# Optimization experiments

Measured on AMD Instinct MI355X. Metric: run time of the kernel, lower is better.

The kernel has to match this reference:

```python
import jax, jax.numpy as jnp
import numpy as np

N_NODES = 10000
N_EDGES = 640000
IN_CH, HID, OUT_CH = 128, 128, 64


def _gcn_conv(x, edge_index, edge_weight, W, b, n_nodes):
    # PyG GCNConv (default add_self_loops=True, normalize=True, bias=True):
    #   A_hat = A + I ; D = rowsum(A_hat) ; norm_e = D^-1/2[src] * w_e * D^-1/2[dst]
    #   out[dst] += norm_e * (x @ W)[src] ; out += b
    src, dst = edge_index[0], edge_index[1]
    loop = jnp.arange(n_nodes, dtype=edge_index.dtype)
    src = jnp.concatenate([src, loop])
    dst = jnp.concatenate([dst, loop])
    w = jnp.concatenate([edge_weight, jnp.ones((n_nodes,), edge_weight.dtype)])
    deg = jax.ops.segment_sum(w, dst, num_segments=n_nodes)  # scatter on col
    dinv = jnp.where(deg > 0, jax.lax.rsqrt(deg), 0.0).astype(x.dtype)
    norm = dinv[src] * w * dinv[dst]  # [E+N]
    xw = x @ W  # dense GEMM [N, out]
    msg = norm[:, None] * xw[src]  # gather + scale [E+N, out]
    out = jax.ops.segment_sum(msg, dst, num_segments=n_nodes)  # scatter-add
    return out + b


def setup_inputs() -> dict:
    key = jax.random.key(0)
    ks = jax.random.split(key, 8)
    x = jax.random.normal(ks[0], (N_NODES, IN_CH), dtype=jnp.float32)
    edge_index = jax.random.randint(ks[1], (2, N_EDGES), 0, N_NODES, dtype=jnp.int64)
    edge_weight = jax.random.uniform(ks[2], (N_EDGES,), dtype=jnp.float32)
    W1 = jax.random.normal(ks[3], (IN_CH, HID), dtype=jnp.float32) * 0.05
    b1 = jnp.zeros((HID,), jnp.float32)
    W2 = jax.random.normal(ks[4], (HID, OUT_CH), dtype=jnp.float32) * 0.05
    b2 = jnp.zeros((OUT_CH,), jnp.float32)
    return {"x": x, "edge_index": edge_index, "edge_weight": edge_weight,
            "W1": W1, "b1": b1, "W2": W2, "b2": b2}


def reference(x, edge_index, edge_weight, W1, b1, W2, b2):
    h = _gcn_conv(x, edge_index, edge_weight, W1, b1, N_NODES)
    h = jax.nn.relu(h)
    out = _gcn_conv(h, edge_index, edge_weight, W2, b2, N_NODES)
    return out
```

## Files before the change

kernel.cpp:

```cpp
#include <hip/hip_runtime.h>
#include <math.h>

#define N_NODES 10000
#define N_EDGES 640000
#define K_DIM   128
#define OUT_CH  64
#define ELLW    192

#define CHUNKS  128
#define CHUNK_E 5000
#define GB      313

typedef unsigned long long ull;
typedef unsigned int uint;
typedef unsigned short ushort;
typedef unsigned char uchar;

#define FIXED_SCALE 262144.0f


__device__ __forceinline__ float bf_lo(uint u) {
    return __uint_as_float(u << 16);
}
__device__ __forceinline__ float bf_hi(uint u) {
    return __uint_as_float(u & 0xffff0000u);
}
__device__ __forceinline__ ushort f2bf(float v) {
    uint u = __float_as_uint(v);
    uint r = u + 0x7fffu + ((u >> 16) & 1u);
    return (ushort)(r >> 16);
}

template <int NCOL>
__device__ void gemm_body(const float* __restrict__ A, const float* __restrict__ B,
                          ushort* __restrict__ C, int blk, int M,
                          float* sA , float* sB ) {
    constexpr int K = 128;
    constexpr int TM = 32;
    constexpr int KT = 32;
    constexpr int R = 256 / NCOL;
    constexpr int RPT = TM / R;
    int tid = threadIdx.x;
    int c = tid % NCOL;
    int rr = tid / NCOL;
    int row0 = blk * TM;
    float acc[RPT];
#pragma unroll
    for (int r = 0; r < RPT; ++r) acc[r] = 0.0f;

    for (int k0 = 0; k0 < K; k0 += KT) {
        for (int i = tid; i < TM * KT; i += 256) {
            int r = i / KT, k = i % KT;
            int gr = row0 + r;
            sA[r * (KT + 1) + k] = (gr < M) ? A[gr * K + k0 + k] : 0.0f;
        }
        for (int i = tid; i < KT * NCOL; i += 256) {
            int k = i / NCOL, cc = i % NCOL;
            sB[k * NCOL + cc] = B[(k0 + k) * NCOL + cc];
        }
        __syncthreads();
#pragma unroll
        for (int k = 0; k < KT; ++k) {
            float b = sB[k * NCOL + c];
#pragma unroll
            for (int r = 0; r < RPT; ++r)
                acc[r] += sA[(rr * RPT + r) * (KT + 1) + k] * b;
        }
        __syncthreads();
    }
#pragma unroll
    for (int r = 0; r < RPT; ++r) {
        int gr = row0 + rr * RPT + r;
        if (gr < M) C[gr * NCOL + c] = f2bf(acc[r]);
    }
}

__global__ __launch_bounds__(256) void preA_gemm1_kernel(const int* __restrict__ ei,
                                                         const float* __restrict__ ew,
                                                         uchar* __restrict__ rank8,
                                                         uint* __restrict__ sd32,
                                                         uint* __restrict__ blockcnt,
                                                         const float* __restrict__ x,
                                                         const float* __restrict__ W1,
                                                         ushort* __restrict__ xw1b) {
    __shared__ uint smem[N_NODES];
    if (blockIdx.x < CHUNKS) {
        const int c = blockIdx.x;
        const int tid = threadIdx.x;
        __shared__ int sflag;
        if (tid == 0) sflag = 0;
        for (int i = tid; i < N_NODES; i += 256) smem[i] = 0u;
        __syncthreads();
        int a = (tid < 64) ? ei[2 * (c * CHUNK_E + tid) + 1] : 0;
        if (a) atomicOr(&sflag, 1);
        __syncthreads();
        const int f = sflag;
        const ull* ei64 = (const ull*)ei;
        for (int k = tid; k < CHUNK_E; k += 256) {
            int e = c * CHUNK_E + k;
            int s, d;
            if (f) { s = ei[e];        d = ei[N_EDGES + e]; }
            else   { s = (int)ei64[e]; d = (int)ei64[N_EDGES + e]; }
            float w = ew[e];
            uint fx = (uint)(w * FIXED_SCALE + 0.5f);
            uint old = atomicAdd(&smem[d], (1u << 24) | fx);
            rank8[e] = (uchar)(old >> 24);
            sd32[e] = ((uint)d << 16) | (uint)s;
        }
        __syncthreads();
        for (int i = tid; i < N_NODES; i += 256)
            blockcnt[c * N_NODES + i] = smem[i];
    } else {
        float* sA = (float*)smem;
        float* sB = sA + 32 * 33;
        gemm_body<128>(x, W1, xw1b, blockIdx.x - CHUNKS, N_NODES, sA, sB);
    }
}

__global__ __launch_bounds__(256) void scanB_kernel(const uint* __restrict__ blockcnt,
                                                    uchar* __restrict__ base8,
                                                    int* __restrict__ cnt_arr,
                                                    float* __restrict__ dinv) {
    int n = blockIdx.x * 256 + threadIdx.x;
    if (n >= N_NODES) return;
    uint wsum = 0;
    int run = 0;
#pragma unroll 8
    for (int c = 0; c < CHUNKS; ++c) {
        uint v = blockcnt[c * N_NODES + n];
        base8[c * N_NODES + n] = (uchar)run;
        run += (int)(v >> 24);
        wsum += v & 0xffffffu;
    }
    cnt_arr[n] = run;
    float dg = 1.0f + (float)wsum * (1.0f / FIXED_SCALE);
    dinv[n] = (float)(1.0 / sqrt((double)dg));
}

#define FILL_SPLIT 4
#define FILL_PART  (CHUNK_E / FILL_SPLIT)
__global__ __launch_bounds__(256) void fillC_kernel(const uint* __restrict__ sd32,
                                                    const float* __restrict__ ew,
                                                    const uchar* __restrict__ rank8,
                                                    const uchar* __restrict__ base8,
                                                    const float* __restrict__ dinv,
                                                    ull* __restrict__ epack) {
    const int c = blockIdx.x / FILL_SPLIT;
    const int p = blockIdx.x % FILL_SPLIT;
    const int k0 = p * FILL_PART;
    for (int k = k0 + threadIdx.x; k < k0 + FILL_PART; k += 256) {
        int e = c * CHUNK_E + k;
        uint sd = sd32[e];
        int s = (int)(sd & 0xffffu);
        int d = (int)(sd >> 16);
        float nrm = dinv[s] * ew[e] * dinv[d];
        int slot = (int)base8[c * N_NODES + d] + (int)rank8[e];
        if (slot < ELLW)
            epack[d * ELLW + slot] = ((ull)__float_as_uint(nrm) << 32) | (ull)(uint)s;
    }
}

__global__ __launch_bounds__(256) void gemm2_kernel(const float* __restrict__ A,
                                                    const float* __restrict__ B,
                                                    ushort* __restrict__ C) {
    __shared__ float sA[32 * 33];
    __shared__ float sB[32 * 64];
    gemm_body<64>(A, B, C, blockIdx.x, N_NODES, sA, sB);
}

__global__ __launch_bounds__(64) void agg1_kernel(const ushort* __restrict__ xwb,
                                                  const ull* __restrict__ epack,
                                                  const int* __restrict__ cnt_arr,
                                                  const float* __restrict__ dinv,
                                                  const float* __restrict__ bias,
                                                  float* __restrict__ out) {
    const uint* __restrict__ xw32 = (const uint*)xwb;
    int node = blockIdx.x;
    int l = threadIdx.x;
    int cnt = __builtin_amdgcn_readfirstlane(cnt_arr[node]);
    if (cnt > ELLW) cnt = ELLW;
    float dn = dinv[node];
    float d2 = dn * dn;
    uint su = xw32[node * 64 + l];
    float acc0 = d2 * bf_lo(su);
    float acc1 = d2 * bf_hi(su);
    const ull* ep = epack + (long)node * ELLW;
#pragma unroll 8
    for (int j = 0; j < cnt; ++j) {
        ull v = ep[j];
        uint s = (uint)v;
        float n = __uint_as_float((uint)(v >> 32));
        uint u = xw32[s * 64 + l];
        acc0 = fmaf(n, bf_lo(u), acc0);
        acc1 = fmaf(n, bf_hi(u), acc1);
    }
    float2 bb = ((const float2*)bias)[l];
    float2 o;
    o.x = fmaxf(acc0 + bb.x, 0.0f);
    o.y = fmaxf(acc1 + bb.y, 0.0f);
    ((float2*)out)[node * 64 + l] = o;
}

__global__ __launch_bounds__(64) void agg2_kernel(const ushort* __restrict__ xwb,
                                                  const ull* __restrict__ epack,
                                                  const int* __restrict__ cnt_arr,
                                                  const float* __restrict__ dinv,
                                                  const float* __restrict__ bias,
                                                  float* __restrict__ out) {
    const uint* __restrict__ xw32 = (const uint*)xwb;
    int A = blockIdx.x * 2;
    int B = A + 1;
    int lane = threadIdx.x;
    int half = lane >> 5;
    int q = lane & 31;
    int cntA = __builtin_amdgcn_readfirstlane(cnt_arr[A]);
    int cntB = __builtin_amdgcn_readfirstlane(cnt_arr[B]);
    if (cntA > ELLW) cntA = ELLW;
    if (cntB > ELLW) cntB = ELLW;
    float dnA = dinv[A], dnB = dinv[B];
    int myn = half ? B : A;
    int mycnt = half ? cntB : cntA;
    float dn = half ? dnB : dnA;
    float d2 = dn * dn;
    uint su = xw32[myn * 32 + q];
    float acc0 = d2 * bf_lo(su);
    float acc1 = d2 * bf_hi(su);
    const ull* epA = epack + (long)A * ELLW;
    const ull* epB = epack + (long)B * ELLW;
    int mx = cntA > cntB ? cntA : cntB;
#pragma unroll 4
    for (int j = 0; j < mx; ++j) {
        ull vA = epA[j];
        ull vB = epB[j];
        ull v = half ? vB : vA;
        uint s = (uint)v & 0xffffu;
        float n = (j < mycnt) ? __uint_as_float((uint)(v >> 32)) : 0.0f;
        uint u = xw32[s * 32 + q];
        acc0 = fmaf(n, bf_lo(u), acc0);
        acc1 = fmaf(n, bf_hi(u), acc1);
    }
    float2 bb = ((const float2*)bias)[q];
    float2 o;
    o.x = acc0 + bb.x;
    o.y = acc1 + bb.y;
    ((float2*)out)[myn * 32 + q] = o;
}

extern "C" void kernel_launch(void* const* d_in, const int* in_sizes, int n_in,
                              void* d_out, int out_size, void* d_ws, size_t ws_size,
                              hipStream_t stream) {
    const float* x  = (const float*)d_in[0];
    const int*   ei = (const int*)d_in[1];
    const float* ew = (const float*)d_in[2];
    const float* W1 = (const float*)d_in[3];
    const float* b1 = (const float*)d_in[4];
    const float* W2 = (const float*)d_in[5];
    const float* b2 = (const float*)d_in[6];
    float* out = (float*)d_out;

    char* ws = (char*)d_ws;
    ushort* xw1b    = (ushort*)(ws + 0);
    float*  h       = (float*) (ws + 2560000);
    ushort* xw2b    = (ushort*)(ws + 7680000);
    ull*    epack   = (ull*)   (ws + 8960000);
    uint*   blockcnt= (uint*)  (ws + 24320000);
    uchar*  base8   = (uchar*) (ws + 29440000);
    uchar*  rank8   = (uchar*) (ws + 30720000);
    uint*   sd32    = (uint*)  (ws + 31360000);
    int*    cnt_arr = (int*)   (ws + 33920000);
    float*  dinv    = (float*) (ws + 33960000);

    preA_gemm1_kernel<<<CHUNKS + GB, 256, 0, stream>>>(ei, ew, rank8, sd32, blockcnt, x, W1, xw1b);
    scanB_kernel<<<(N_NODES + 255) / 256, 256, 0, stream>>>(blockcnt, base8, cnt_arr, dinv);
    fillC_kernel<<<CHUNKS * FILL_SPLIT, 256, 0, stream>>>(sd32, ew, rank8, base8, dinv, epack);
    agg1_kernel<<<N_NODES, 64, 0, stream>>>(xw1b, epack, cnt_arr, dinv, b1, h);
    gemm2_kernel<<<GB, 256, 0, stream>>>(h, W2, xw2b);
    agg2_kernel<<<N_NODES / 2, 64, 0, stream>>>(xw2b, epack, cnt_arr, dinv, b2, out);
}
```

Before: 167.9 us.

## Fuse all GCN stages into one persistent kernel with grid barriers

Replaces six kernel launches with a single persistent kernel of 512 blocks that runs every phase (edge counting plus GEMM1, scan, ELL fill, aggregation 1, GEMM2, aggregation 2), separated by atomic-counter grid barriers. It also stores the hidden activations as bf16 instead of fp32 to halve that traffic. The aim is to remove launch gaps and tail effects between stages. In exchange, the grid-stride loops may load-balance worse than per-node blocks, the barriers rely on all 512 blocks being co-resident, and the extra bf16 rounding of the hidden layer adds error.

```diff
diff --git a/kernel.cpp b/kernel.cpp
--- a/kernel.cpp
+++ b/kernel.cpp
@@ -3,13 +3,13 @@
 
 #define N_NODES 10000
 #define N_EDGES 640000
-#define K_DIM   128
 #define OUT_CH  64
 #define ELLW    192
 
 #define CHUNKS  128
 #define CHUNK_E 5000
 #define GB      313
+#define NBLOCKS 512
 
 typedef unsigned long long ull;
 typedef unsigned int uint;
@@ -19,74 +19,42 @@
 #define FIXED_SCALE 262144.0f
 
 
-__device__ __forceinline__ float bf_lo(uint u) {
-    return __uint_as_float(u << 16);
-}
-__device__ __forceinline__ float bf_hi(uint u) {
-    return __uint_as_float(u & 0xffff0000u);
-}
+__device__ __forceinline__ float bf_lo(uint u) { return __uint_as_float(u << 16); }
+__device__ __forceinline__ float bf_hi(uint u) { return __uint_as_float(u & 0xffff0000u); }
 __device__ __forceinline__ ushort f2bf(float v) {
     uint u = __float_as_uint(v);
     uint r = u + 0x7fffu + ((u >> 16) & 1u);
     return (ushort)(r >> 16);
 }
 
-template <int NCOL>
-__device__ void gemm_body(const float* __restrict__ A, const float* __restrict__ B,
-                          ushort* __restrict__ C, int blk, int M,
-                          float* sA , float* sB ) {
-    constexpr int K = 128;
-    constexpr int TM = 32;
-    constexpr int KT = 32;
-    constexpr int R = 256 / NCOL;
-    constexpr int RPT = TM / R;
-    int tid = threadIdx.x;
-    int c = tid % NCOL;
-    int rr = tid / NCOL;
-    int row0 = blk * TM;
-    float acc[RPT];
-#pragma unroll
-    for (int r = 0; r < RPT; ++r) acc[r] = 0.0f;
-
-    for (int k0 = 0; k0 < K; k0 += KT) {
-        for (int i = tid; i < TM * KT; i += 256) {
-            int r = i / KT, k = i % KT;
-            int gr = row0 + r;
-            sA[r * (KT + 1) + k] = (gr < M) ? A[gr * K + k0 + k] : 0.0f;
-        }
-        for (int i = tid; i < KT * NCOL; i += 256) {
-            int k = i / NCOL, cc = i % NCOL;
-            sB[k * NCOL + cc] = B[(k0 + k) * NCOL + cc];
-        }
-        __syncthreads();
-#pragma unroll
-        for (int k = 0; k < KT; ++k) {
-            float b = sB[k * NCOL + c];
-#pragma unroll
-            for (int r = 0; r < RPT; ++r)
-                acc[r] += sA[(rr * RPT + r) * (KT + 1) + k] * b;
-        }
-        __syncthreads();
-    }
-#pragma unroll
-    for (int r = 0; r < RPT; ++r) {
-        int gr = row0 + rr * RPT + r;
-        if (gr < M) C[gr * NCOL + c] = f2bf(acc[r]);
-    }
-}
-
-__global__ __launch_bounds__(256) void preA_gemm1_kernel(const int* __restrict__ ei,
-                                                         const float* __restrict__ ew,
-                                                         uchar* __restrict__ rank8,
-                                                         uint* __restrict__ sd32,
-                                                         uint* __restrict__ blockcnt,
-                                                         const float* __restrict__ x,
-                                                         const float* __restrict__ W1,
-                                                         ushort* __restrict__ xw1b) {
-    __shared__ uint smem[N_NODES];
-    if (blockIdx.x < CHUNKS) {
-        const int c = blockIdx.x;
-        const int tid = threadIdx.x;
+__device__ __forceinline__ void grid_barrier(int* __restrict__ bar, int idx) {
+    __syncthreads();
+    if (threadIdx.x == 0) {
+        __threadfence();
+        int prev = __hip_atomic_fetch_add(&bar[idx], 1, __ATOMIC_ACQ_REL,
+                                          __HIP_MEMORY_SCOPE_AGENT);
+        if (prev + 1 < NBLOCKS) {
+            while (__hip_atomic_load(&bar[idx], __ATOMIC_ACQUIRE,
+                                     __HIP_MEMORY_SCOPE_AGENT) < NBLOCKS)
+                __builtin_amdgcn_s_sleep(2);
+        }
+        __threadfence();
+    }
+    __syncthreads();
+}
+
+__global__ __launch_bounds__(64) void init_bar_kernel(int* __restrict__ bar) {
+    if (threadIdx.x < 8) bar[threadIdx.x] = 0;
+}
+
+__device__ void phase1(int bid, const int* __restrict__ ei, const float* __restrict__ ew,
+                       uchar* __restrict__ rank8, uint* __restrict__ sd32,
+                       uint* __restrict__ blockcnt, const float* __restrict__ x,
+                       const float* __restrict__ W1, ushort* __restrict__ xw1b,
+                       uint* smem) {
+    const int tid = threadIdx.x;
+    if (bid < CHUNKS) {
+        const int c = bid;
         __shared__ int sflag;
         if (tid == 0) sflag = 0;
         for (int i = tid; i < N_NODES; i += 256) smem[i] = 0u;
@@ -110,49 +78,71 @@
         __syncthreads();
         for (int i = tid; i < N_NODES; i += 256)
             blockcnt[c * N_NODES + i] = smem[i];
-    } else {
+    } else if (bid < CHUNKS + GB) {
+        constexpr int K = 128, TM = 32, KT = 32, NCOL = 128, RPT = 16;
         float* sA = (float*)smem;
-        float* sB = sA + 32 * 33;
-        gemm_body<128>(x, W1, xw1b, blockIdx.x - CHUNKS, N_NODES, sA, sB);
-    }
-}
-
-__global__ __launch_bounds__(256) void scanB_kernel(const uint* __restrict__ blockcnt,
-                                                    uchar* __restrict__ base8,
-                                                    int* __restrict__ cnt_arr,
-                                                    float* __restrict__ dinv) {
-    int n = blockIdx.x * 256 + threadIdx.x;
-    if (n >= N_NODES) return;
+        float* sB = sA + TM * (KT + 1);
+        int blk = bid - CHUNKS;
+        int c = tid % NCOL, rr = tid / NCOL;
+        int row0 = blk * TM;
+        float acc[RPT];
+#pragma unroll
+        for (int r = 0; r < RPT; ++r) acc[r] = 0.0f;
+        for (int k0 = 0; k0 < K; k0 += KT) {
+            for (int i = tid; i < TM * KT; i += 256) {
+                int r = i / KT, k = i % KT;
+                int gr = row0 + r;
+                sA[r * (KT + 1) + k] = (gr < N_NODES) ? x[gr * K + k0 + k] : 0.0f;
+            }
+            for (int i = tid; i < KT * NCOL; i += 256) {
+                int k = i / NCOL, cc = i % NCOL;
+                sB[k * NCOL + cc] = W1[(k0 + k) * NCOL + cc];
+            }
+            __syncthreads();
+#pragma unroll
+            for (int k = 0; k < KT; ++k) {
+                float b = sB[k * NCOL + c];
+#pragma unroll
+                for (int r = 0; r < RPT; ++r)
+                    acc[r] += sA[(rr * RPT + r) * (KT + 1) + k] * b;
+            }
+            __syncthreads();
+        }
+#pragma unroll
+        for (int r = 0; r < RPT; ++r) {
+            int gr = row0 + rr * RPT + r;
+            if (gr < N_NODES) xw1b[gr * NCOL + c] = f2bf(acc[r]);
+        }
+    }
+}
+
+__device__ void phase2(int gid, const uint* __restrict__ blockcnt,
+                       uchar* __restrict__ base8, int* __restrict__ cnt_arr,
+                       float* __restrict__ dinv) {
+    if (gid >= N_NODES) return;
     uint wsum = 0;
     int run = 0;
 #pragma unroll 8
     for (int c = 0; c < CHUNKS; ++c) {
-        uint v = blockcnt[c * N_NODES + n];
-        base8[c * N_NODES + n] = (uchar)run;
+        uint v = blockcnt[c * N_NODES + gid];
+        base8[c * N_NODES + gid] = (uchar)run;
         run += (int)(v >> 24);
         wsum += v & 0xffffffu;
     }
-    cnt_arr[n] = run;
+    cnt_arr[gid] = run;
     float dg = 1.0f + (float)wsum * (1.0f / FIXED_SCALE);
-    dinv[n] = (float)(1.0 / sqrt((double)dg));
-}
-
-#define FILL_SPLIT 4
-#define FILL_PART  (CHUNK_E / FILL_SPLIT)
-__global__ __launch_bounds__(256) void fillC_kernel(const uint* __restrict__ sd32,
-                                                    const float* __restrict__ ew,
-                                                    const uchar* __restrict__ rank8,
-                                                    const uchar* __restrict__ base8,
-                                                    const float* __restrict__ dinv,
-                                                    ull* __restrict__ epack) {
-    const int c = blockIdx.x / FILL_SPLIT;
-    const int p = blockIdx.x % FILL_SPLIT;
-    const int k0 = p * FILL_PART;
-    for (int k = k0 + threadIdx.x; k < k0 + FILL_PART; k += 256) {
-        int e = c * CHUNK_E + k;
+    dinv[gid] = (float)(1.0 / sqrt((double)dg));
+}
+
+__device__ void phase3(int gid, int stride, const uint* __restrict__ sd32,
+                       const float* __restrict__ ew, const uchar* __restrict__ rank8,
+                       const uchar* __restrict__ base8, const float* __restrict__ dinv,
+                       ull* __restrict__ epack) {
+    for (int e = gid; e < N_EDGES; e += stride) {
         uint sd = sd32[e];
         int s = (int)(sd & 0xffffu);
         int d = (int)(sd >> 16);
+        int c = e / CHUNK_E;
         float nrm = dinv[s] * ew[e] * dinv[d];
         int slot = (int)base8[c * N_NODES + d] + (int)rank8[e];
         if (slot < ELLW)
@@ -160,90 +150,153 @@
     }
 }
 
-__global__ __launch_bounds__(256) void gemm2_kernel(const float* __restrict__ A,
-                                                    const float* __restrict__ B,
-                                                    ushort* __restrict__ C) {
-    __shared__ float sA[32 * 33];
-    __shared__ float sB[32 * 64];
-    gemm_body<64>(A, B, C, blockIdx.x, N_NODES, sA, sB);
-}
-
-__global__ __launch_bounds__(64) void agg1_kernel(const ushort* __restrict__ xwb,
-                                                  const ull* __restrict__ epack,
-                                                  const int* __restrict__ cnt_arr,
-                                                  const float* __restrict__ dinv,
-                                                  const float* __restrict__ bias,
-                                                  float* __restrict__ out) {
-    const uint* __restrict__ xw32 = (const uint*)xwb;
-    int node = blockIdx.x;
-    int l = threadIdx.x;
-    int cnt = __builtin_amdgcn_readfirstlane(cnt_arr[node]);
-    if (cnt > ELLW) cnt = ELLW;
-    float dn = dinv[node];
-    float d2 = dn * dn;
-    uint su = xw32[node * 64 + l];
-    float acc0 = d2 * bf_lo(su);
-    float acc1 = d2 * bf_hi(su);
-    const ull* ep = epack + (long)node * ELLW;
+__device__ void phase4(int bid, const ushort* __restrict__ xw1b,
+                       const ull* __restrict__ epack, const int* __restrict__ cnt_arr,
+                       const float* __restrict__ dinv, const float* __restrict__ b1,
+                       uint* __restrict__ hb32) {
+    const uint* __restrict__ xw32 = (const uint*)xw1b;
+    int l = threadIdx.x & 63;
+    int wave = bid * 4 + (threadIdx.x >> 6);
+    int totw = NBLOCKS * 4;
+    for (int node = wave; node < N_NODES; node += totw) {
+        int cnt = __builtin_amdgcn_readfirstlane(cnt_arr[node]);
+        if (cnt > ELLW) cnt = ELLW;
+        float dn = dinv[node];
+        float d2 = dn * dn;
+        uint su = xw32[node * 64 + l];
+        float acc0 = d2 * bf_lo(su);
+        float acc1 = d2 * bf_hi(su);
+        const ull* ep = epack + (long)node * ELLW;
 #pragma unroll 8
-    for (int j = 0; j < cnt; ++j) {
-        ull v = ep[j];
-        uint s = (uint)v;
-        float n = __uint_as_float((uint)(v >> 32));
-        uint u = xw32[s * 64 + l];
-        acc0 = fmaf(n, bf_lo(u), acc0);
-        acc1 = fmaf(n, bf_hi(u), acc1);
-    }
-    float2 bb = ((const float2*)bias)[l];
-    float2 o;
-    o.x = fmaxf(acc0 + bb.x, 0.0f);
-    o.y = fmaxf(acc1 + bb.y, 0.0f);
-    ((float2*)out)[node * 64 + l] = o;
-}
-
-__global__ __launch_bounds__(64) void agg2_kernel(const ushort* __restrict__ xwb,
-                                                  const ull* __restrict__ epack,
-                                                  const int* __restrict__ cnt_arr,
-                                                  const float* __restrict__ dinv,
-                                                  const float* __restrict__ bias,
-                                                  float* __restrict__ out) {
-    const uint* __restrict__ xw32 = (const uint*)xwb;
-    int A = blockIdx.x * 2;
-    int B = A + 1;
-    int lane = threadIdx.x;
+        for (int j = 0; j < cnt; ++j) {
+            ull v = ep[j];
+            uint s = (uint)v;
+            float n = __uint_as_float((uint)(v >> 32));
+            uint u = xw32[s * 64 + l];
+            acc0 = fmaf(n, bf_lo(u), acc0);
+            acc1 = fmaf(n, bf_hi(u), acc1);
+        }
+        float2 bb = ((const float2*)b1)[l];
+        float o0 = fmaxf(acc0 + bb.x, 0.0f);
+        float o1 = fmaxf(acc1 + bb.y, 0.0f);
+        hb32[node * 64 + l] = ((uint)f2bf(o1) << 16) | (uint)f2bf(o0);
+    }
+}
+
+__device__ void phase5(int bid, const uint* __restrict__ hb32,
+                       const float* __restrict__ W2, ushort* __restrict__ xw2b,
+                       uint* smem) {
+    constexpr int K = 128, TM = 32, KT = 32, NCOL = 64, RPT = 8;
+    float* sA = (float*)smem;
+    float* sB = sA + TM * (KT + 1);
+    const int tid = threadIdx.x;
+    int c = tid % NCOL, rr = tid / NCOL;
+    for (int blk = bid; blk < GB; blk += NBLOCKS) {
+        int row0 = blk * TM;
+        float acc[RPT];
+#pragma unroll
+        for (int r = 0; r < RPT; ++r) acc[r] = 0.0f;
+        for (int k0 = 0; k0 < K; k0 += KT) {
+            for (int i = tid; i < TM * (KT / 2); i += 256) {
+                int r = i / (KT / 2), kk = i % (KT / 2);
+                int gr = row0 + r;
+                uint u = (gr < N_NODES) ? hb32[gr * 64 + (k0 >> 1) + kk] : 0u;
+                sA[r * (KT + 1) + 2 * kk]     = bf_lo(u);
+                sA[r * (KT + 1) + 2 * kk + 1] = bf_hi(u);
+            }
+            for (int i = tid; i < KT * NCOL; i += 256) {
+                int k = i / NCOL, cc = i % NCOL;
+                sB[k * NCOL + cc] = W2[(k0 + k) * NCOL + cc];
+            }
+            __syncthreads();
+#pragma unroll
+            for (int k = 0; k < KT; ++k) {
+                float b = sB[k * NCOL + c];
+#pragma unroll
+                for (int r = 0; r < RPT; ++r)
+                    acc[r] += sA[(rr * RPT + r) * (KT + 1) + k] * b;
+            }
+            __syncthreads();
+        }
+#pragma unroll
+        for (int r = 0; r < RPT; ++r) {
+            int gr = row0 + rr * RPT + r;
+            if (gr < N_NODES) xw2b[gr * NCOL + c] = f2bf(acc[r]);
+        }
+    }
+}
+
+__device__ void phase6(int bid, const ushort* __restrict__ xw2b,
+                       const ull* __restrict__ epack, const int* __restrict__ cnt_arr,
+                       const float* __restrict__ dinv, const float* __restrict__ b2,
+                       float* __restrict__ out) {
+    const uint* __restrict__ xw32 = (const uint*)xw2b;
+    int lane = threadIdx.x & 63;
     int half = lane >> 5;
     int q = lane & 31;
-    int cntA = __builtin_amdgcn_readfirstlane(cnt_arr[A]);
-    int cntB = __builtin_amdgcn_readfirstlane(cnt_arr[B]);
-    if (cntA > ELLW) cntA = ELLW;
-    if (cntB > ELLW) cntB = ELLW;
-    float dnA = dinv[A], dnB = dinv[B];
-    int myn = half ? B : A;
-    int mycnt = half ? cntB : cntA;
-    float dn = half ? dnB : dnA;
-    float d2 = dn * dn;
-    uint su = xw32[myn * 32 + q];
-    float acc0 = d2 * bf_lo(su);
-    float acc1 = d2 * bf_hi(su);
-    const ull* epA = epack + (long)A * ELLW;
-    const ull* epB = epack + (long)B * ELLW;
-    int mx = cntA > cntB ? cntA : cntB;
+    int wave = bid * 4 + (threadIdx.x >> 6);
+    int totw = NBLOCKS * 4;
+    for (int pair = wave; pair < N_NODES / 2; pair += totw) {
+        int A = pair * 2, B = A + 1;
+        int cntA = __builtin_amdgcn_readfirstlane(cnt_arr[A]);
+        int cntB = __builtin_amdgcn_readfirstlane(cnt_arr[B]);
+        if (cntA > ELLW) cntA = ELLW;
+        if (cntB > ELLW) cntB = ELLW;
+        int myn = half ? B : A;
+        int mycnt = half ? cntB : cntA;
+        float dn = dinv[myn];
+        float d2 = dn * dn;
+        uint su = xw32[myn * 32 + q];
+        float acc0 = d2 * bf_lo(su);
+        float acc1 = d2 * bf_hi(su);
+        const ull* epA = epack + (long)A * ELLW;
+        const ull* epB = epack + (long)B * ELLW;
+        int mx = cntA > cntB ? cntA : cntB;
 #pragma unroll 4
-    for (int j = 0; j < mx; ++j) {
-        ull vA = epA[j];
-        ull vB = epB[j];
-        ull v = half ? vB : vA;
-        uint s = (uint)v & 0xffffu;
-        float n = (j < mycnt) ? __uint_as_float((uint)(v >> 32)) : 0.0f;
-        uint u = xw32[s * 32 + q];
-        acc0 = fmaf(n, bf_lo(u), acc0);
-        acc1 = fmaf(n, bf_hi(u), acc1);
-    }
-    float2 bb = ((const float2*)bias)[q];
-    float2 o;
-    o.x = acc0 + bb.x;
-    o.y = acc1 + bb.y;
-    ((float2*)out)[myn * 32 + q] = o;
+        for (int j = 0; j < mx; ++j) {
+            ull vA = epA[j];
+            ull vB = epB[j];
+            ull v = half ? vB : vA;
+            uint s = (uint)v & 0xffffu;
+            float n = (j < mycnt) ? __uint_as_float((uint)(v >> 32)) : 0.0f;
+            uint u = xw32[s * 32 + q];
+            acc0 = fmaf(n, bf_lo(u), acc0);
+            acc1 = fmaf(n, bf_hi(u), acc1);
+        }
+        float2 bb = ((const float2*)b2)[q];
+        float2 o;
+        o.x = acc0 + bb.x;
+        o.y = acc1 + bb.y;
+        ((float2*)out)[myn * 32 + q] = o;
+    }
+}
+
+__global__ __launch_bounds__(256, 2) void mega_kernel(const int* ei, const float* ew,
+                                                      const float* x, const float* W1,
+                                                      const float* b1, const float* W2,
+                                                      const float* b2, float* out,
+                                                      ushort* xw1b, uint* hb32,
+                                                      ushort* xw2b, ull* epack,
+                                                      uint* blockcnt, uchar* base8,
+                                                      uchar* rank8, uint* sd32,
+                                                      int* cnt_arr, float* dinv,
+                                                      int* bar) {
+    __shared__ uint smem[10240];
+    const int bid = blockIdx.x;
+    const int gid = bid * 256 + threadIdx.x;
+    const int stride = NBLOCKS * 256;
+
+    phase1(bid, ei, ew, rank8, sd32, blockcnt, x, W1, xw1b, smem);
+    grid_barrier(bar, 0);
+    phase2(gid, blockcnt, base8, cnt_arr, dinv);
+    grid_barrier(bar, 1);
+    phase3(gid, stride, sd32, ew, rank8, base8, dinv, epack);
+    grid_barrier(bar, 2);
+    phase4(bid, xw1b, epack, cnt_arr, dinv, b1, hb32);
+    grid_barrier(bar, 3);
+    phase5(bid, hb32, W2, xw2b, smem);
+    grid_barrier(bar, 4);
+    phase6(bid, xw2b, epack, cnt_arr, dinv, b2, out);
 }
 
 extern "C" void kernel_launch(void* const* d_in, const int* in_sizes, int n_in,
@@ -260,20 +313,19 @@
 
     char* ws = (char*)d_ws;
     ushort* xw1b    = (ushort*)(ws + 0);
-    float*  h       = (float*) (ws + 2560000);
-    ushort* xw2b    = (ushort*)(ws + 7680000);
-    ull*    epack   = (ull*)   (ws + 8960000);
-    uint*   blockcnt= (uint*)  (ws + 24320000);
-    uchar*  base8   = (uchar*) (ws + 29440000);
-    uchar*  rank8   = (uchar*) (ws + 30720000);
-    uint*   sd32    = (uint*)  (ws + 31360000);
-    int*    cnt_arr = (int*)   (ws + 33920000);
-    float*  dinv    = (float*) (ws + 33960000);
-
-    preA_gemm1_kernel<<<CHUNKS + GB, 256, 0, stream>>>(ei, ew, rank8, sd32, blockcnt, x, W1, xw1b);
-    scanB_kernel<<<(N_NODES + 255) / 256, 256, 0, stream>>>(blockcnt, base8, cnt_arr, dinv);
-    fillC_kernel<<<CHUNKS * FILL_SPLIT, 256, 0, stream>>>(sd32, ew, rank8, base8, dinv, epack);
-    agg1_kernel<<<N_NODES, 64, 0, stream>>>(xw1b, epack, cnt_arr, dinv, b1, h);
-    gemm2_kernel<<<GB, 256, 0, stream>>>(h, W2, xw2b);
-    agg2_kernel<<<N_NODES / 2, 64, 0, stream>>>(xw2b, epack, cnt_arr, dinv, b2, out);
-}
+    uint*   hb32    = (uint*)  (ws + 2560000);
+    ushort* xw2b    = (ushort*)(ws + 5120000);
+    ull*    epack   = (ull*)   (ws + 6400000);
+    uint*   blockcnt= (uint*)  (ws + 21760000);
+    uchar*  base8   = (uchar*) (ws + 26880000);
+    uchar*  rank8   = (uchar*) (ws + 28160000);
+    uint*   sd32    = (uint*)  (ws + 28800000);
+    int*    cnt_arr = (int*)   (ws + 31360000);
+    float*  dinv    = (float*) (ws + 31400000);
+    int*    bar     = (int*)   (ws + 31440000);
+
+    init_bar_kernel<<<1, 64, 0, stream>>>(bar);
+    mega_kernel<<<NBLOCKS, 256, 0, stream>>>(ei, ew, x, W1, b1, W2, b2, out,
+                                             xw1b, hb32, xw2b, epack, blockcnt,
+                                             base8, rank8, sd32, cnt_arr, dinv, bar);
+}
```

New measurement: 629.3 us. 3.75x slower.
